# Optimization experiments

Hardware: AMD Instinct MI355X
Metric: run time of the kernel (lower is better)

## Reference

```python
import jax, jax.numpy as jnp
import numpy as np

N_EMBD = 2048
N_HEAD = 32
N_KV_HEAD = 8
HEAD_DIM = N_EMBD // N_HEAD  # 64
N_REP = N_HEAD // N_KV_HEAD  # 4
B, T = 2, 2048


def setup_inputs() -> dict:
    key = jax.random.key(0)
    ks = jax.random.split(key, 9)
    s = 1.0 / np.sqrt(N_EMBD)
    kv_dim = N_KV_HEAD * HEAD_DIM
    return {
        "x": jax.random.normal(ks[0], (B, T, N_EMBD), dtype=jnp.float32),
        "Wq": jax.random.normal(ks[1], (N_EMBD, N_EMBD), dtype=jnp.float32) * s,
        "bq": jax.random.normal(ks[2], (N_EMBD,), dtype=jnp.float32) * 0.01,
        "Wk": jax.random.normal(ks[3], (N_EMBD, kv_dim), dtype=jnp.float32) * s,
        "bk": jax.random.normal(ks[4], (kv_dim,), dtype=jnp.float32) * 0.01,
        "Wv": jax.random.normal(ks[5], (N_EMBD, kv_dim), dtype=jnp.float32) * s,
        "bv": jax.random.normal(ks[6], (kv_dim,), dtype=jnp.float32) * 0.01,
        "Wo": jax.random.normal(ks[7], (N_EMBD, N_EMBD), dtype=jnp.float32) * s,
        "bo": jax.random.normal(ks[8], (N_EMBD,), dtype=jnp.float32) * 0.01,
    }


def reference(x, Wq, bq, Wk, bk, Wv, bv, Wo, bo):
    Bsz, Tlen, C = x.shape
    # projections
    q = (x @ Wq + bq).reshape(Bsz, Tlen, N_HEAD, HEAD_DIM).transpose(0, 2, 1, 3)   # [B,H,T,d]
    k = (x @ Wk + bk).reshape(Bsz, Tlen, N_KV_HEAD, HEAD_DIM).transpose(0, 2, 1, 3)  # [B,Hkv,T,d]
    v = (x @ Wv + bv).reshape(Bsz, Tlen, N_KV_HEAD, HEAD_DIM).transpose(0, 2, 1, 3)
    # repeat_interleave KV heads to match query heads
    k = jnp.repeat(k, N_REP, axis=1)  # [B,H,T,d]
    v = jnp.repeat(v, N_REP, axis=1)
    # causal SDPA
    scale = 1.0 / jnp.sqrt(jnp.asarray(HEAD_DIM, dtype=x.dtype))
    scores = jnp.einsum('bhqd,bhkd->bhqk', q, k) * scale  # [B,H,T,T]
    causal = jnp.tril(jnp.ones((Tlen, Tlen), dtype=bool))
    scores = jnp.where(causal, scores, jnp.asarray(-jnp.inf, dtype=scores.dtype))
    attn = jax.nn.softmax(scores, axis=-1)
    y = jnp.einsum('bhqk,bhkd->bhqd', attn, v)  # [B,H,T,d]
    y = y.transpose(0, 2, 1, 3).reshape(Bsz, Tlen, C)
    return y @ Wo + bo
```

## Files before the change

### kernel.cpp

```cpp
#include <hip/hip_runtime.h>
#include <hip/hip_bf16.h>

#define B_SZ   2
#define T_SEQ  2048
#define C_EMB  2048
#define KV_DIM 512

typedef __bf16 bf16x8 __attribute__((ext_vector_type(8)));
typedef __bf16 bf16x4 __attribute__((ext_vector_type(4)));
typedef float  f32x4  __attribute__((ext_vector_type(4)));
typedef float  f32x16 __attribute__((ext_vector_type(16)));
typedef unsigned int u32;

typedef __attribute__((address_space(1))) const unsigned int gu32;
typedef __attribute__((address_space(3))) unsigned int lu32;
__device__ __forceinline__ void gload16(const void* g, void* l) {
  __builtin_amdgcn_global_load_lds((gu32*)g, (lu32*)l, 16, 0, 0);
}

__global__ __launch_bounds__(256) void cast_f32_bf16(const float* __restrict__ in,
                                                     __bf16* __restrict__ out, int n8) {
  int i = blockIdx.x * 256 + threadIdx.x;
  if (i < n8) {
    const float4* p = (const float4*)(in + (size_t)i * 8);
    float4 a = p[0], b = p[1];
    bf16x8 o;
    o[0] = (__bf16)a.x; o[1] = (__bf16)a.y; o[2] = (__bf16)a.z; o[3] = (__bf16)a.w;
    o[4] = (__bf16)b.x; o[5] = (__bf16)b.y; o[6] = (__bf16)b.z; o[7] = (__bf16)b.w;
    *(bf16x8*)(out + (size_t)i * 8) = o;
  }
}

__global__ __launch_bounds__(256) void transpose_cast_kernel(const float* __restrict__ in,
                                                             __bf16* __restrict__ out,
                                                             int R, int C) {
  __shared__ float tile[64][65];
  int c0 = blockIdx.x * 64, r0 = blockIdx.y * 64;
  int tid = threadIdx.x;
#pragma unroll
  for (int i = 0; i < 4; i++) {
    int idx = tid + i * 256;
    int row = idx >> 4;
    int c4  = (idx & 15) * 4;
    float4 v = *(const float4*)&in[(size_t)(r0 + row) * C + c0 + c4];
    tile[row][c4 + 0] = v.x; tile[row][c4 + 1] = v.y;
    tile[row][c4 + 2] = v.z; tile[row][c4 + 3] = v.w;
  }
  __syncthreads();
#pragma unroll
  for (int i = 0; i < 4; i++) {
    int idx = tid + i * 256;
    int col = idx >> 4;
    int r4  = (idx & 15) * 4;
    bf16x4 o;
    o[0] = (__bf16)tile[r4 + 0][col];
    o[1] = (__bf16)tile[r4 + 1][col];
    o[2] = (__bf16)tile[r4 + 2][col];
    o[3] = (__bf16)tile[r4 + 3][col];
    *(bf16x4*)&out[(size_t)(c0 + col) * R + r0 + r4] = o;
  }
}

__global__ __launch_bounds__(256) void concat_bias(const float* __restrict__ bq,
                                                   const float* __restrict__ bk,
                                                   const float* __restrict__ bv,
                                                   float* __restrict__ bcat) {
  int i = blockIdx.x * 256 + threadIdx.x;
  if (i < 3072) {
    float v = (i < 2048) ? bq[i] : (i < 2560 ? bk[i - 2048] : bv[i - 2560]);
    bcat[i] = v;
  }
}

template <int MODE>
__global__ __launch_bounds__(256) void gemm_bt(const __bf16* __restrict__ A,
                                               const __bf16* __restrict__ Bt,
                                               const float* __restrict__ bias,
                                               void* __restrict__ out0,
                                               __bf16* __restrict__ outK,
                                               __bf16* __restrict__ outV,
                                               int M, int N, int K) {
  __shared__ __bf16 As[128 * 32];
  __shared__ __bf16 Bs[128 * 32];
  int tid  = threadIdx.x;
  int lane = tid & 63, wave = tid >> 6;
  int wr = wave >> 1, wc = wave & 1;
  int la = lane & 15, kg = lane >> 4;
  int m0 = blockIdx.x * 128, n0 = blockIdx.y * 128;

  f32x4 acc[4][4];
#pragma unroll
  for (int i = 0; i < 4; i++)
#pragma unroll
    for (int j = 0; j < 4; j++)
#pragma unroll
      for (int r = 0; r < 4; r++) acc[i][j][r] = 0.f;

  int s0 = tid, s1 = tid + 256;
  const __bf16* ga0 = A  + (size_t)(m0 + (s0 >> 2)) * K + (s0 & 3) * 8;
  const __bf16* ga1 = A  + (size_t)(m0 + (s1 >> 2)) * K + (s1 & 3) * 8;
  const __bf16* gb0 = Bt + (size_t)(n0 + (s0 >> 2)) * K + (s0 & 3) * 8;
  const __bf16* gb1 = Bt + (size_t)(n0 + (s1 >> 2)) * K + (s1 & 3) * 8;
  __bf16* lA0 = As + (size_t)(0 * 256 + wave * 64) * 8;
  __bf16* lA1 = As + (size_t)(1 * 256 + wave * 64) * 8;
  __bf16* lB0 = Bs + (size_t)(0 * 256 + wave * 64) * 8;
  __bf16* lB1 = Bs + (size_t)(1 * 256 + wave * 64) * 8;

  for (int k0 = 0; k0 < K; k0 += 32) {
    gload16(ga0 + k0, lA0);
    gload16(ga1 + k0, lA1);
    gload16(gb0 + k0, lB0);
    gload16(gb1 + k0, lB1);
    __syncthreads();
    bf16x8 af[4], bfr[4];
#pragma unroll
    for (int i = 0; i < 4; i++) af[i]  = *(const bf16x8*)&As[(size_t)(wr * 64 + i * 16 + la) * 32 + kg * 8];
#pragma unroll
    for (int j = 0; j < 4; j++) bfr[j] = *(const bf16x8*)&Bs[(size_t)(wc * 64 + j * 16 + la) * 32 + kg * 8];
#pragma unroll
    for (int i = 0; i < 4; i++)
#pragma unroll
      for (int j = 0; j < 4; j++)
        acc[i][j] = __builtin_amdgcn_mfma_f32_16x16x32_bf16(af[i], bfr[j], acc[i][j], 0, 0, 0);
    __syncthreads();
  }

#pragma unroll
  for (int i = 0; i < 4; i++) {
    int rowb = m0 + wr * 64 + i * 16 + kg * 4;
#pragma unroll
    for (int j = 0; j < 4; j++) {
      int col = n0 + wc * 64 + j * 16 + la;
      float bv = bias[col];
#pragma unroll
      for (int r = 0; r < 4; r++) {
        float v = acc[i][j][r] + bv;
        if (MODE == 2) {
          ((float*)out0)[(size_t)(rowb + r) * N + col] = v;
        } else {
          if (n0 < 2048)      ((__bf16*)out0)[(size_t)(rowb + r) * 2048 + col] = (__bf16)(v * 0.18033688f);
          else if (n0 < 2560) outK[(size_t)(rowb + r) * 512 + (col - 2048)] = (__bf16)v;
          else                outV[(size_t)(col - 2560) * M + rowb + r] = (__bf16)v;
        }
      }
    }
  }
}

__global__ __launch_bounds__(128) void attn_kernel(const __bf16* __restrict__ Q,
                                                   const __bf16* __restrict__ K,
                                                   const __bf16* __restrict__ Vt,
                                                   __bf16* __restrict__ Y) {
  __shared__ __bf16 Ylds[2][32][72];
  const int M = B_SZ * T_SEQ;
  int tid = threadIdx.x;
  int wv = tid >> 6, l = tid & 63;
  int qcol = l & 31, hh = l >> 5;
  int g = blockIdx.x;
  int qt = 31 - (g >> 6);
  int bh = g & 63;
  int b = bh >> 5, hq = bh & 31, kvh = hq >> 2;
  int q0w = qt * 64 + wv * 32;

  const __bf16* qrow = Q + (size_t)(b * T_SEQ + q0w + qcol) * C_EMB + hq * 64;
  bf16x8 qf[4];
#pragma unroll
  for (int c = 0; c < 4; c++) qf[c] = *(const bf16x8*)(qrow + c * 16 + hh * 8);

  f32x16 acc0, acc1;
#pragma unroll
  for (int r = 0; r < 16; r++) { acc0[r] = 0.f; acc1[r] = 0.f; }
  float m_run = -1e30f, l_run = 0.f;

  const __bf16* kbase = K + (size_t)(b * T_SEQ + qcol) * KV_DIM + kvh * 64 + hh * 8;
  const __bf16* vb0 = Vt + (size_t)(kvh * 64 + qcol) * M + (size_t)b * T_SEQ + 4 * hh;
  const __bf16* vb1 = vb0 + (size_t)32 * M;

  bf16x8 kf[4];
#pragma unroll
  for (int c = 0; c < 4; c++) kf[c] = *(const bf16x8*)(kbase + c * 16);

  for (int kb = 0; kb <= q0w; kb += 32) {
    f32x16 s;
#pragma unroll
    for (int r = 0; r < 16; r++) s[r] = 0.f;
    __builtin_amdgcn_s_setprio(1);
#pragma unroll
    for (int c = 0; c < 4; c++)
      s = __builtin_amdgcn_mfma_f32_32x32x16_bf16(kf[c], qf[c], s, 0, 0, 0);
    __builtin_amdgcn_s_setprio(0);
    {
      int nkb = (kb + 32 <= q0w) ? kb + 32 : 0;
      const __bf16* nk = kbase + (size_t)nkb * KV_DIM;
#pragma unroll
      for (int c = 0; c < 4; c++) kf[c] = *(const bf16x8*)(nk + c * 16);
    }
    union { bf16x4 h[2]; bf16x8 v; } va00, va01, va10, va11;
    va00.h[0] = *(const bf16x4*)(vb0 + kb);
    va00.h[1] = *(const bf16x4*)(vb0 + kb + 8);
    va01.h[0] = *(const bf16x4*)(vb0 + kb + 16);
    va01.h[1] = *(const bf16x4*)(vb0 + kb + 24);
    va10.h[0] = *(const bf16x4*)(vb1 + kb);
    va10.h[1] = *(const bf16x4*)(vb1 + kb + 8);
    va11.h[0] = *(const bf16x4*)(vb1 + kb + 16);
    va11.h[1] = *(const bf16x4*)(vb1 + kb + 24);
    if (kb == q0w) {
#pragma unroll
      for (int r = 0; r < 16; r++) {
        int kr = (r & 3) + 8 * (r >> 2) + 4 * hh;
        s[r] = (kr <= qcol) ? s[r] : -1e30f;
      }
    }
    float m01 = fmaxf(s[0], s[1]),  m23 = fmaxf(s[2], s[3]);
    float m45 = fmaxf(s[4], s[5]),  m67 = fmaxf(s[6], s[7]);
    float m89 = fmaxf(s[8], s[9]),  mab = fmaxf(s[10], s[11]);
    float mcd = fmaxf(s[12], s[13]), mef = fmaxf(s[14], s[15]);
    float mloc = fmaxf(fmaxf(fmaxf(m01, m23), fmaxf(m45, m67)),
                       fmaxf(fmaxf(m89, mab), fmaxf(mcd, mef)));
    mloc = fmaxf(mloc, __shfl_xor(mloc, 32, 64));
    if (__any(mloc > m_run + 6.0f)) {
      float mnew = fmaxf(m_run, mloc);
      float corr = exp2f(m_run - mnew);
      l_run *= corr;
#pragma unroll
      for (int r = 0; r < 16; r++) { acc0[r] *= corr; acc1[r] *= corr; }
      m_run = mnew;
    }
#pragma unroll
    for (int r = 0; r < 16; r++) s[r] = exp2f(s[r] - m_run);
    l_run += (((s[0] + s[1]) + (s[2] + s[3])) + ((s[4] + s[5]) + (s[6] + s[7])))
           + (((s[8] + s[9]) + (s[10] + s[11])) + ((s[12] + s[13]) + (s[14] + s[15])));
    union { u32 u[4]; bf16x8 v; } w0u, w1u;
#pragma unroll
    for (int j = 0; j < 4; j++) {
      union { __bf16 b2[2]; u32 u; } p0, p1;
      p0.b2[0] = (__bf16)s[2 * j];     p0.b2[1] = (__bf16)s[2 * j + 1];
      p1.b2[0] = (__bf16)s[8 + 2 * j]; p1.b2[1] = (__bf16)s[9 + 2 * j];
      w0u.u[j] = p0.u;
      w1u.u[j] = p1.u;
    }
    __builtin_amdgcn_s_setprio(1);
    acc0 = __builtin_amdgcn_mfma_f32_32x32x16_bf16(va00.v, w0u.v, acc0, 0, 0, 0);
    acc0 = __builtin_amdgcn_mfma_f32_32x32x16_bf16(va01.v, w1u.v, acc0, 0, 0, 0);
    acc1 = __builtin_amdgcn_mfma_f32_32x32x16_bf16(va10.v, w0u.v, acc1, 0, 0, 0);
    acc1 = __builtin_amdgcn_mfma_f32_32x32x16_bf16(va11.v, w1u.v, acc1, 0, 0, 0);
    __builtin_amdgcn_s_setprio(0);
  }

  l_run += __shfl_xor(l_run, 32, 64);
  float inv = 1.0f / l_run;
  __bf16 (*slab)[72] = Ylds[wv];
#pragma unroll
  for (int r = 0; r < 16; r++) {
    int drow = (r & 3) + 8 * (r >> 2) + 4 * hh;
    slab[qcol][drow]      = (__bf16)(acc0[r] * inv);
    slab[qcol][32 + drow] = (__bf16)(acc1[r] * inv);
  }
  __syncthreads();
  __bf16* yrow = Y + (size_t)(b * T_SEQ + q0w + qcol) * C_EMB + hq * 64 + hh * 32;
#pragma unroll
  for (int c = 0; c < 4; c++)
    *(bf16x8*)(yrow + c * 8) = *(const bf16x8*)&slab[qcol][hh * 32 + c * 8];
}

extern "C" void kernel_launch(void* const* d_in, const int* in_sizes, int n_in,
                              void* d_out, int out_size, void* d_ws, size_t ws_size,
                              hipStream_t stream) {
  const float* x  = (const float*)d_in[0];
  const float* Wq = (const float*)d_in[1];
  const float* bq = (const float*)d_in[2];
  const float* Wk = (const float*)d_in[3];
  const float* bk = (const float*)d_in[4];
  const float* Wv = (const float*)d_in[5];
  const float* bv = (const float*)d_in[6];
  const float* Wo = (const float*)d_in[7];
  const float* bo = (const float*)d_in[8];
  float* out = (float*)d_out;

  const int M = B_SZ * T_SEQ;

  char* w = (char*)d_ws;
  __bf16* xb   = (__bf16*)w; w += (size_t)M * C_EMB * 2;
  __bf16* Wall = (__bf16*)w; w += (size_t)3072 * C_EMB * 2;
  __bf16* Wot  = (__bf16*)w; w += (size_t)C_EMB * C_EMB * 2;
  float*  bcat = (float*)w;  w += (size_t)3072 * 4;
  __bf16* qb   = (__bf16*)w; w += (size_t)M * C_EMB * 2;
  __bf16* kbf  = (__bf16*)w; w += (size_t)M * KV_DIM * 2;
  __bf16* vbt  = (__bf16*)w; w += (size_t)KV_DIM * M * 2;
  __bf16* yb   = (__bf16*)w; w += (size_t)M * C_EMB * 2;

  cast_f32_bf16<<<(M * C_EMB / 8 + 255) / 256, 256, 0, stream>>>(x, xb, M * C_EMB / 8);

  transpose_cast_kernel<<<dim3(C_EMB / 64, C_EMB / 64), 256, 0, stream>>>(Wq, Wall, C_EMB, C_EMB);
  transpose_cast_kernel<<<dim3(KV_DIM / 64, C_EMB / 64), 256, 0, stream>>>(Wk, Wall + (size_t)2048 * C_EMB, C_EMB, KV_DIM);
  transpose_cast_kernel<<<dim3(KV_DIM / 64, C_EMB / 64), 256, 0, stream>>>(Wv, Wall + (size_t)2560 * C_EMB, C_EMB, KV_DIM);
  transpose_cast_kernel<<<dim3(C_EMB / 64, C_EMB / 64), 256, 0, stream>>>(Wo, Wot, C_EMB, C_EMB);
  concat_bias<<<12, 256, 0, stream>>>(bq, bk, bv, bcat);

  gemm_bt<1><<<dim3(M / 128, 3072 / 128), 256, 0, stream>>>(xb, Wall, bcat, qb, kbf, vbt, M, 3072, C_EMB);

  attn_kernel<<<dim3(2048), 128, 0, stream>>>(qb, kbf, vbt, yb);

  gemm_bt<2><<<dim3(M / 128, C_EMB / 128), 256, 0, stream>>>(yb, Wot, bo, out, nullptr, nullptr, M, C_EMB, C_EMB);
}
```

Before: 441.9 us.

## Pair causal query tiles per wave and permute V layout for vector loads

```diff
diff --git a/kernel.cpp b/kernel.cpp
--- a/kernel.cpp
+++ b/kernel.cpp
@@ -125,9 +125,11 @@
     __syncthreads();
   }
 
+  int kgsw = ((kg & 1) << 1) | (kg >> 1);
 #pragma unroll
   for (int i = 0; i < 4; i++) {
-    int rowb = m0 + wr * 64 + i * 16 + kg * 4;
+    int rowb  = m0 + wr * 64 + i * 16 + kg * 4;
+    int rowbV = m0 + wr * 64 + i * 16 + kgsw * 4;
 #pragma unroll
     for (int j = 0; j < 4; j++) {
       int col = n0 + wc * 64 + j * 16 + la;
@@ -140,7 +142,7 @@
         } else {
           if (n0 < 2048)      ((__bf16*)out0)[(size_t)(rowb + r) * 2048 + col] = (__bf16)(v * 0.18033688f);
           else if (n0 < 2560) outK[(size_t)(rowb + r) * 512 + (col - 2048)] = (__bf16)v;
-          else                outV[(size_t)(col - 2560) * M + rowb + r] = (__bf16)v;
+          else                outV[(size_t)(col - 2560) * M + rowbV + r] = (__bf16)v;
         }
       }
     }
@@ -157,110 +159,109 @@
   int wv = tid >> 6, l = tid & 63;
   int qcol = l & 31, hh = l >> 5;
   int g = blockIdx.x;
-  int qt = 31 - (g >> 6);
-  int bh = g & 63;
+  int swz = (g & 7) * 128 + (g >> 3);
+  int bh = swz >> 4, pi2 = swz & 15;
+  int pi = pi2 * 2 + wv;
   int b = bh >> 5, hq = bh & 31, kvh = hq >> 2;
-  int q0w = qt * 64 + wv * 32;
-
-  const __bf16* qrow = Q + (size_t)(b * T_SEQ + q0w + qcol) * C_EMB + hq * 64;
-  bf16x8 qf[4];
-#pragma unroll
-  for (int c = 0; c < 4; c++) qf[c] = *(const bf16x8*)(qrow + c * 16 + hh * 8);
-
-  f32x16 acc0, acc1;
-#pragma unroll
-  for (int r = 0; r < 16; r++) { acc0[r] = 0.f; acc1[r] = 0.f; }
-  float m_run = -1e30f, l_run = 0.f;
 
   const __bf16* kbase = K + (size_t)(b * T_SEQ + qcol) * KV_DIM + kvh * 64 + hh * 8;
-  const __bf16* vb0 = Vt + (size_t)(kvh * 64 + qcol) * M + (size_t)b * T_SEQ + 4 * hh;
+  const __bf16* vb0 = Vt + (size_t)(kvh * 64 + qcol) * M + (size_t)b * T_SEQ + hh * 8;
   const __bf16* vb1 = vb0 + (size_t)32 * M;
-
-  bf16x8 kf[4];
-#pragma unroll
-  for (int c = 0; c < 4; c++) kf[c] = *(const bf16x8*)(kbase + c * 16);
-
-  for (int kb = 0; kb <= q0w; kb += 32) {
-    f32x16 s;
-#pragma unroll
-    for (int r = 0; r < 16; r++) s[r] = 0.f;
-    __builtin_amdgcn_s_setprio(1);
+  __bf16 (*slab)[72] = Ylds[wv];
+
+  for (int halfi = 0; halfi < 2; ++halfi) {
+    int qt = halfi ? (63 - pi) : pi;
+    int q0 = qt * 32;
+
+    const __bf16* qrow = Q + (size_t)(b * T_SEQ + q0 + qcol) * C_EMB + hq * 64;
+    bf16x8 qf[4];
+#pragma unroll
+    for (int c = 0; c < 4; c++) qf[c] = *(const bf16x8*)(qrow + c * 16 + hh * 8);
+
+    f32x16 acc0, acc1;
+#pragma unroll
+    for (int r = 0; r < 16; r++) { acc0[r] = 0.f; acc1[r] = 0.f; }
+    float m_run = -1e30f, l_run = 0.f;
+
+    bf16x8 kf[4];
+#pragma unroll
+    for (int c = 0; c < 4; c++) kf[c] = *(const bf16x8*)(kbase + c * 16);
+
+    for (int kb = 0; kb <= q0; kb += 32) {
+      f32x16 s;
+#pragma unroll
+      for (int r = 0; r < 16; r++) s[r] = 0.f;
+      __builtin_amdgcn_s_setprio(1);
+#pragma unroll
+      for (int c = 0; c < 4; c++)
+        s = __builtin_amdgcn_mfma_f32_32x32x16_bf16(kf[c], qf[c], s, 0, 0, 0);
+      __builtin_amdgcn_s_setprio(0);
+      {
+        int nkb = (kb + 32 <= q0) ? kb + 32 : 0;
+        const __bf16* nk = kbase + (size_t)nkb * KV_DIM;
+#pragma unroll
+        for (int c = 0; c < 4; c++) kf[c] = *(const bf16x8*)(nk + c * 16);
+      }
+      bf16x8 vf0 = *(const bf16x8*)(vb0 + kb);
+      bf16x8 vf1 = *(const bf16x8*)(vb0 + kb + 16);
+      bf16x8 vf2 = *(const bf16x8*)(vb1 + kb);
+      bf16x8 vf3 = *(const bf16x8*)(vb1 + kb + 16);
+      if (kb == q0) {
+#pragma unroll
+        for (int r = 0; r < 16; r++) {
+          int kr = (r & 3) + 8 * (r >> 2) + 4 * hh;
+          s[r] = (kr <= qcol) ? s[r] : -1e30f;
+        }
+      }
+      float m01 = fmaxf(s[0], s[1]),  m23 = fmaxf(s[2], s[3]);
+      float m45 = fmaxf(s[4], s[5]),  m67 = fmaxf(s[6], s[7]);
+      float m89 = fmaxf(s[8], s[9]),  mab = fmaxf(s[10], s[11]);
+      float mcd = fmaxf(s[12], s[13]), mef = fmaxf(s[14], s[15]);
+      float mloc = fmaxf(fmaxf(fmaxf(m01, m23), fmaxf(m45, m67)),
+                         fmaxf(fmaxf(m89, mab), fmaxf(mcd, mef)));
+      mloc = fmaxf(mloc, __shfl_xor(mloc, 32, 64));
+      if (__any(mloc > m_run + 6.0f)) {
+        float mnew = fmaxf(m_run, mloc);
+        float corr = exp2f(m_run - mnew);
+        l_run *= corr;
+#pragma unroll
+        for (int r = 0; r < 16; r++) { acc0[r] *= corr; acc1[r] *= corr; }
+        m_run = mnew;
+      }
+#pragma unroll
+      for (int r = 0; r < 16; r++) s[r] = exp2f(s[r] - m_run);
+      l_run += (((s[0] + s[1]) + (s[2] + s[3])) + ((s[4] + s[5]) + (s[6] + s[7])))
+             + (((s[8] + s[9]) + (s[10] + s[11])) + ((s[12] + s[13]) + (s[14] + s[15])));
+      union { u32 u[4]; bf16x8 v; } w0u, w1u;
+#pragma unroll
+      for (int j = 0; j < 4; j++) {
+        union { __bf16 b2[2]; u32 u; } p0, p1;
+        p0.b2[0] = (__bf16)s[2 * j];     p0.b2[1] = (__bf16)s[2 * j + 1];
+        p1.b2[0] = (__bf16)s[8 + 2 * j]; p1.b2[1] = (__bf16)s[9 + 2 * j];
+        w0u.u[j] = p0.u;
+        w1u.u[j] = p1.u;
+      }
+      __builtin_amdgcn_s_setprio(1);
+      acc0 = __builtin_amdgcn_mfma_f32_32x32x16_bf16(vf0, w0u.v, acc0, 0, 0, 0);
+      acc0 = __builtin_amdgcn_mfma_f32_32x32x16_bf16(vf1, w1u.v, acc0, 0, 0, 0);
+      acc1 = __builtin_amdgcn_mfma_f32_32x32x16_bf16(vf2, w0u.v, acc1, 0, 0, 0);
+      acc1 = __builtin_amdgcn_mfma_f32_32x32x16_bf16(vf3, w1u.v, acc1, 0, 0, 0);
+      __builtin_amdgcn_s_setprio(0);
+    }
+
+    l_run += __shfl_xor(l_run, 32, 64);
+    float inv = 1.0f / l_run;
+#pragma unroll
+    for (int r = 0; r < 16; r++) {
+      int drow = (r & 3) + 8 * (r >> 2) + 4 * hh;
+      slab[qcol][drow]      = (__bf16)(acc0[r] * inv);
+      slab[qcol][32 + drow] = (__bf16)(acc1[r] * inv);
+    }
+    __bf16* yrow = Y + (size_t)(b * T_SEQ + q0 + qcol) * C_EMB + hq * 64 + hh * 32;
 #pragma unroll
     for (int c = 0; c < 4; c++)
-      s = __builtin_amdgcn_mfma_f32_32x32x16_bf16(kf[c], qf[c], s, 0, 0, 0);
-    __builtin_amdgcn_s_setprio(0);
-    {
-      int nkb = (kb + 32 <= q0w) ? kb + 32 : 0;
-      const __bf16* nk = kbase + (size_t)nkb * KV_DIM;
-#pragma unroll
-      for (int c = 0; c < 4; c++) kf[c] = *(const bf16x8*)(nk + c * 16);
-    }
-    union { bf16x4 h[2]; bf16x8 v; } va00, va01, va10, va11;
-    va00.h[0] = *(const bf16x4*)(vb0 + kb);
-    va00.h[1] = *(const bf16x4*)(vb0 + kb + 8);
-    va01.h[0] = *(const bf16x4*)(vb0 + kb + 16);
-    va01.h[1] = *(const bf16x4*)(vb0 + kb + 24);
-    va10.h[0] = *(const bf16x4*)(vb1 + kb);
-    va10.h[1] = *(const bf16x4*)(vb1 + kb + 8);
-    va11.h[0] = *(const bf16x4*)(vb1 + kb + 16);
-    va11.h[1] = *(const bf16x4*)(vb1 + kb + 24);
-    if (kb == q0w) {
-#pragma unroll
-      for (int r = 0; r < 16; r++) {
-        int kr = (r & 3) + 8 * (r >> 2) + 4 * hh;
-        s[r] = (kr <= qcol) ? s[r] : -1e30f;
-      }
-    }
-    float m01 = fmaxf(s[0], s[1]),  m23 = fmaxf(s[2], s[3]);
-    float m45 = fmaxf(s[4], s[5]),  m67 = fmaxf(s[6], s[7]);
-    float m89 = fmaxf(s[8], s[9]),  mab = fmaxf(s[10], s[11]);
-    float mcd = fmaxf(s[12], s[13]), mef = fmaxf(s[14], s[15]);
-    float mloc = fmaxf(fmaxf(fmaxf(m01, m23), fmaxf(m45, m67)),
-                       fmaxf(fmaxf(m89, mab), fmaxf(mcd, mef)));
-    mloc = fmaxf(mloc, __shfl_xor(mloc, 32, 64));
-    if (__any(mloc > m_run + 6.0f)) {
-      float mnew = fmaxf(m_run, mloc);
-      float corr = exp2f(m_run - mnew);
-      l_run *= corr;
-#pragma unroll
-      for (int r = 0; r < 16; r++) { acc0[r] *= corr; acc1[r] *= corr; }
-      m_run = mnew;
-    }
-#pragma unroll
-    for (int r = 0; r < 16; r++) s[r] = exp2f(s[r] - m_run);
-    l_run += (((s[0] + s[1]) + (s[2] + s[3])) + ((s[4] + s[5]) + (s[6] + s[7])))
-           + (((s[8] + s[9]) + (s[10] + s[11])) + ((s[12] + s[13]) + (s[14] + s[15])));
-    union { u32 u[4]; bf16x8 v; } w0u, w1u;
-#pragma unroll
-    for (int j = 0; j < 4; j++) {
-      union { __bf16 b2[2]; u32 u; } p0, p1;
-      p0.b2[0] = (__bf16)s[2 * j];     p0.b2[1] = (__bf16)s[2 * j + 1];
-      p1.b2[0] = (__bf16)s[8 + 2 * j]; p1.b2[1] = (__bf16)s[9 + 2 * j];
-      w0u.u[j] = p0.u;
-      w1u.u[j] = p1.u;
-    }
-    __builtin_amdgcn_s_setprio(1);
-    acc0 = __builtin_amdgcn_mfma_f32_32x32x16_bf16(va00.v, w0u.v, acc0, 0, 0, 0);
-    acc0 = __builtin_amdgcn_mfma_f32_32x32x16_bf16(va01.v, w1u.v, acc0, 0, 0, 0);
-    acc1 = __builtin_amdgcn_mfma_f32_32x32x16_bf16(va10.v, w0u.v, acc1, 0, 0, 0);
-    acc1 = __builtin_amdgcn_mfma_f32_32x32x16_bf16(va11.v, w1u.v, acc1, 0, 0, 0);
-    __builtin_amdgcn_s_setprio(0);
-  }
-
-  l_run += __shfl_xor(l_run, 32, 64);
-  float inv = 1.0f / l_run;
-  __bf16 (*slab)[72] = Ylds[wv];
-#pragma unroll
-  for (int r = 0; r < 16; r++) {
-    int drow = (r & 3) + 8 * (r >> 2) + 4 * hh;
-    slab[qcol][drow]      = (__bf16)(acc0[r] * inv);
-    slab[qcol][32 + drow] = (__bf16)(acc1[r] * inv);
-  }
-  __syncthreads();
-  __bf16* yrow = Y + (size_t)(b * T_SEQ + q0w + qcol) * C_EMB + hq * 64 + hh * 32;
-#pragma unroll
-  for (int c = 0; c < 4; c++)
-    *(bf16x8*)(yrow + c * 8) = *(const bf16x8*)&slab[qcol][hh * 32 + c * 8];
+      *(bf16x8*)(yrow + c * 8) = *(const bf16x8*)&slab[qcol][hh * 32 + c * 8];
+  }
 }
 
 extern "C" void kernel_launch(void* const* d_in, const int* in_sizes, int n_in,
@@ -299,7 +300,7 @@
 
   gemm_bt<1><<<dim3(M / 128, 3072 / 128), 256, 0, stream>>>(xb, Wall, bcat, qb, kbf, vbt, M, 3072, C_EMB);
 
-  attn_kernel<<<dim3(2048), 128, 0, stream>>>(qb, kbf, vbt, yb);
+  attn_kernel<<<dim3(1024), 128, 0, stream>>>(qb, kbf, vbt, yb);
 
   gemm_bt<2><<<dim3(M / 128, C_EMB / 128), 256, 0, stream>>>(yb, Wot, bo, out, nullptr, nullptr, M, C_EMB, C_EMB);
 }
```

New measurement: 377.8 us. 1.17x faster.
